# Performance work log

Hardware: AMD Instinct MI355X
Metric: run time of the kernel (lower is better)

## Reference

```python
import jax, jax.numpy as jnp
import numpy as np

IN_F = 175
HID = 1024
OUT_F = 175


def setup_inputs() -> dict:
    key = jax.random.key(0)
    ks = jax.random.split(key, 16)
    B, T = 128, 200
    s = 0.02
    w = lambda k, shape: (jax.random.normal(k, shape, jnp.float32) * s)
    return {
        "real_seq": jax.random.normal(ks[0], (B, T, IN_F), jnp.float32),
        "W_ih1": w(ks[1], (4 * HID, IN_F)), "W_hh1": w(ks[2], (4 * HID, HID)),
        "b_ih1": w(ks[3], (4 * HID,)), "b_hh1": w(ks[4], (4 * HID,)),
        "W_ih2": w(ks[5], (4 * HID, HID)), "W_hh2": w(ks[6], (4 * HID, HID)),
        "b_ih2": w(ks[7], (4 * HID,)), "b_hh2": w(ks[8], (4 * HID,)),
        "W_ih3": w(ks[9], (4 * HID, HID)), "W_hh3": w(ks[10], (4 * HID, HID)),
        "b_ih3": w(ks[11], (4 * HID,)), "b_hh3": w(ks[12], (4 * HID,)),
        "W_dec": w(ks[13], (OUT_F, HID)), "b_dec": w(ks[14], (OUT_F,)),
    }


def _condition_mask(seq_len, condition_num=5, groundtruth_num=5):
    gt = np.ones((100, groundtruth_num))
    con = np.zeros((100, condition_num))
    lst = np.concatenate((gt, con), 1).reshape(-1)[:seq_len]
    return jnp.asarray(lst.astype(bool))


def _lstm_cell(x, h, c, Wih, Whh, bih, bhh):
    # PyTorch LSTMCell: gate order i, f, g, o
    gates = x @ Wih.T + h @ Whh.T + bih + bhh
    i, f, g, o = jnp.split(gates, 4, axis=-1)
    c_new = jax.nn.sigmoid(f) * c + jax.nn.sigmoid(i) * jnp.tanh(g)
    h_new = jax.nn.sigmoid(o) * jnp.tanh(c_new)
    return h_new, c_new


def reference(real_seq, W_ih1, W_hh1, b_ih1, b_hh1,
              W_ih2, W_hh2, b_ih2, b_hh2,
              W_ih3, W_hh3, b_ih3, b_hh3,
              W_dec, b_dec):
    B, T, _ = real_seq.shape
    H = W_hh1.shape[1]
    Fo = W_dec.shape[0]
    cond = _condition_mask(T)
    z = jnp.zeros((B, H), real_seq.dtype)
    carry0 = (z, z, z, z, z, z, jnp.zeros((B, Fo), real_seq.dtype))

    def step(carry, xs):
        h0, h1, h2, c0, c1, c2, out_frame = carry
        x_t, use_gt = xs
        in_frame = jnp.where(use_gt, x_t, out_frame)
        nh0, nc0 = _lstm_cell(in_frame, h0, c0, W_ih1, W_hh1, b_ih1, b_hh1)
        # NOTE: source feeds the PREVIOUS h0 / h1 to layers 2 / 3 (faithful)
        nh1, nc1 = _lstm_cell(h0, h1, c1, W_ih2, W_hh2, b_ih2, b_hh2)
        nh2, nc2 = _lstm_cell(h1, h2, c2, W_ih3, W_hh3, b_ih3, b_hh3)
        out = nh2 @ W_dec.T + b_dec
        return (nh0, nh1, nh2, nc0, nc1, nc2, out), out

    _, outs = jax.lax.scan(step, carry0,
                           (jnp.transpose(real_seq, (1, 0, 2)), cond))
    # [T, B, Fo] -> [B, T*Fo] (matches torch.cat along dim 1 per step)
    return jnp.transpose(outs, (1, 0, 2)).reshape(B, T * Fo)
```

## Files before the change

### kernel.cpp

```cpp
#include <hip/hip_runtime.h>

#define B_ 128
#define T_ 200
#define INF_ 175
#define INFP_ 192
#define H_ 1024
#define G4_ 4096
#define OUTF_ 175
#define BH3_ (3 * B_ * H_)
#define NCELL 192
#define NDEC 22
#define NWORK (NCELL + NDEC)
#define NBLK (NWORK + 1)
#define SP 16

typedef __bf16 bf16x8 __attribute__((ext_vector_type(8)));
typedef float f32x4 __attribute__((ext_vector_type(4)));

__device__ __attribute__((aligned(16))) __bf16 g_Wih1p[G4_ * INFP_];
__device__ __attribute__((aligned(16))) __bf16 g_Whh1[G4_ * H_];
__device__ __attribute__((aligned(16))) __bf16 g_Wih2[G4_ * H_];
__device__ __attribute__((aligned(16))) __bf16 g_Whh2[G4_ * H_];
__device__ __attribute__((aligned(16))) __bf16 g_Wih3[G4_ * H_];
__device__ __attribute__((aligned(16))) __bf16 g_Whh3[G4_ * H_];
__device__ __attribute__((aligned(16))) __bf16 g_Wdec[OUTF_ * H_];
__device__ float g_bsum[3 * G4_];
__device__ float g_bdec[OUTF_];
__device__ __attribute__((aligned(16))) __bf16 g_h[2][BH3_];
__device__ __attribute__((aligned(16))) __bf16 g_infp[B_ * INFP_];
__device__ int g_isf32;
__device__ int g_flags[256 * SP];
__device__ int g_dflags[32 * SP];
__device__ int g_gen8[8 * SP];
__device__ int g_iready8[8 * SP];

__device__ __forceinline__ f32x4 mfma_bf16(bf16x8 a, bf16x8 b, f32x4 c) {
    return __builtin_amdgcn_mfma_f32_16x16x32_bf16(a, b, c, 0, 0, 0);
}
__device__ __forceinline__ bf16x8 ld8(const __bf16* p) {
    return *reinterpret_cast<const bf16x8*>(p);
}
__device__ __forceinline__ float sigm(float x) { return 1.f / (1.f + expf(-x)); }
__device__ __forceinline__ float rdf(const void* p, long i, int f32) {
    return f32 ? ((const float*)p)[i] : (float)((const __bf16*)p)[i];
}
__device__ __forceinline__ unsigned short bf2u(__bf16 v) {
    union { __bf16 b; unsigned short u; } c; c.b = v; return c.u;
}

__device__ __forceinline__ void spin_rmw(int* addr, int target, int iters) {
    for (int it = 0; it < iters; ++it) {
        if (__hip_atomic_fetch_max(addr, 0, __ATOMIC_RELAXED, __HIP_MEMORY_SCOPE_AGENT) >= target)
            break;
        __builtin_amdgcn_s_sleep(1);
    }
    (void)__hip_atomic_load(addr, __ATOMIC_ACQUIRE, __HIP_MEMORY_SCOPE_AGENT);
}

__global__ void detect_k(const unsigned int* __restrict__ xw) {
    __shared__ int cnt;
    if (threadIdx.x == 0) cnt = 0;
    __syncthreads();
    unsigned int w = xw[threadIdx.x];
    int e = (w >> 7) & 0xFF;
    if (e >= 140) atomicAdd(&cnt, 1);
    __syncthreads();
    if (threadIdx.x == 0) g_isf32 = (cnt >= 16) ? 1 : 0;
}

__global__ void prep_k(const void* Wih1, const void* Whh1, const void* Wih2,
                       const void* Whh2, const void* Wih3, const void* Whh3,
                       const void* Wdec, const void* bih1, const void* bhh1,
                       const void* bih2, const void* bhh2, const void* bih3,
                       const void* bhh3, const void* bdec, const void* xseq) {
    const int f = g_isf32;
    const int idx = blockIdx.x * 256 + threadIdx.x;
    const int stride = gridDim.x * 256;
    if (idx < 256 * SP) g_flags[idx] = 0;
    if (idx < 32 * SP) g_dflags[idx] = 0;
    if (idx < 8 * SP) { g_gen8[idx] = 0; g_iready8[idx] = 0; }
    for (int i = idx; i < G4_ * INFP_; i += stride) {
        int n = i / INFP_, k = i - n * INFP_;
        g_Wih1p[i] = (k < INF_) ? (__bf16)rdf(Wih1, (long)n * INF_ + k, f) : (__bf16)0.f;
    }
    for (int i = idx; i < G4_ * H_; i += stride) {
        g_Whh1[i] = (__bf16)rdf(Whh1, i, f);
        g_Wih2[i] = (__bf16)rdf(Wih2, i, f);
        g_Whh2[i] = (__bf16)rdf(Whh2, i, f);
        g_Wih3[i] = (__bf16)rdf(Wih3, i, f);
        g_Whh3[i] = (__bf16)rdf(Whh3, i, f);
    }
    for (int i = idx; i < OUTF_ * H_; i += stride) g_Wdec[i] = (__bf16)rdf(Wdec, i, f);
    for (int i = idx; i < G4_; i += stride) {
        g_bsum[i]           = rdf(bih1, i, f) + rdf(bhh1, i, f);
        g_bsum[G4_ + i]     = rdf(bih2, i, f) + rdf(bhh2, i, f);
        g_bsum[2 * G4_ + i] = rdf(bih3, i, f) + rdf(bhh3, i, f);
    }
    for (int i = idx; i < OUTF_; i += stride) g_bdec[i] = rdf(bdec, i, f);
    for (int i = idx; i < 2 * BH3_; i += stride) (&g_h[0][0])[i] = (__bf16)0.f;
    for (int i = idx; i < B_ * INFP_; i += stride) {
        int b = i / INFP_, k = i - b * INFP_;
        g_infp[i] = (k < INF_) ? (__bf16)rdf(xseq, (long)b * (T_ * INF_) + k, f) : (__bf16)0.f;
    }
}

__device__ __forceinline__ void gridbar_w(int bid, int grp, int target) {
    __syncthreads();
    if (threadIdx.x == 0) {
        __threadfence();
        __hip_atomic_fetch_max(&g_flags[bid * SP], target, __ATOMIC_RELAXED, __HIP_MEMORY_SCOPE_AGENT);
        spin_rmw(&g_gen8[grp * SP], target, 4000);
    }
    __syncthreads();
}

__global__ __launch_bounds__(512, 1) void persist_k(const void* __restrict__ xseq,
                                                    void* __restrict__ dout) {
    __shared__ char s_tile[2][2][16384];
    __shared__ float s_acc[B_ * 4 * 16];
    __shared__ float s_c[B_ * 16];
    __shared__ int s_nf, s_nd;
    const int bid = blockIdx.x;
    const int grp = bid & 7;
    const int tid = threadIdx.x;
    const int lane = tid & 63;
    const int wid = tid >> 6;
    const int rlo = lane & 15, khi = lane >> 4;
    const int f32o = g_isf32;
    const int r7l = rlo & 7;
    const int sw0 = (khi ^ r7l) * 16;
    const int sw1 = ((khi + 4) ^ r7l) * 16;

    if (bid < NCELL) {
        const int L = bid >> 6;
        const int hc0 = (bid & 63) << 4;
        const int op = wid >> 2;
        const int g = wid & 3;
        const float* bs = g_bsum + L * G4_;

        const __bf16* Bm; int K;
        if (op == 0) {
            if (L == 0) { Bm = g_Wih1p; K = INFP_; }
            else        { Bm = (L == 1) ? g_Wih2 : g_Wih3; K = H_; }
        } else {
            Bm = (L == 0) ? g_Whh1 : (L == 1) ? g_Whh2 : g_Whh3; K = H_;
        }
        const __bf16* wp = Bm + (long)(g * H_ + hc0 + rlo) * K + khi * 8;
        bf16x8 wreg[32];
        if (K == INFP_) {
#pragma unroll
            for (int c = 0; c < 6; ++c) wreg[c] = ld8(wp + c * 32);
        } else {
#pragma unroll
            for (int c = 0; c < 32; ++c) wreg[c] = ld8(wp + c * 32);
        }

        const int strow = tid >> 2, stq = tid & 3, str7 = strow & 7;
        auto ldchunk = [&](const __bf16* src, int sA, int k0, bf16x8& v0, bf16x8& v1) {
            const __bf16* pr = src + (long)strow * sA + k0 + stq * 8;
            v0 = ld8(pr);
            v1 = ld8(pr + 32);
        };
        auto wrchunk = [&](char* tile, bf16x8 v0, bf16x8 v1) {
            char* pb = tile + strow * 128;
            *(bf16x8*)(pb + ((stq ^ str7) * 16)) = v0;
            *(bf16x8*)(pb + (((stq + 4) ^ str7) * 16)) = v1;
        };

        for (int i = tid; i < B_ * 16; i += 512) s_c[i] = 0.f;
        __syncthreads();

        for (int p = 0; p < T_; ++p) {
            const __bf16* hin = g_h[p & 1];
            const __bf16* Apx; int sAx, nx;
            if (L == 0) { Apx = g_infp; sAx = INFP_; nx = 3; }
            else        { Apx = hin + (L - 1) * B_ * H_; sAx = H_; nx = 16; }
            const __bf16* Aph = hin + L * B_ * H_;

            if (L == 0 && p > 0) {
                if (tid == 0) spin_rmw(&g_iready8[grp * SP], p, 3000);
                __syncthreads();
            }

            bf16x8 rx0, rx1, rh0, rh1;
            ldchunk(Aph, H_, 0, rh0, rh1);
            ldchunk(Apx, sAx, 0, rx0, rx1);
            wrchunk(&s_tile[0][1][0], rh0, rh1);
            wrchunk(&s_tile[0][0][0], rx0, rx1);
            ldchunk(Aph, H_, 64, rh0, rh1);
            ldchunk(Apx, sAx, 64, rx0, rx1);
            __syncthreads();

            f32x4 acc[8] = {};
            int buf = 0;
#pragma unroll
            for (int i = 0; i < 16; ++i) {
                if (i < 15) wrchunk(&s_tile[buf ^ 1][1][0], rh0, rh1);
                if (i + 1 < nx) wrchunk(&s_tile[buf ^ 1][0][0], rx0, rx1);
                if (i < 14) ldchunk(Aph, H_, (i + 2) * 64, rh0, rh1);
                if (i + 2 < nx) ldchunk(Apx, sAx, (i + 2) * 64, rx0, rx1);
                if (op == 1 || i < nx) {
                    const char* tb = &s_tile[buf][op][0];
#pragma unroll
                    for (int mf = 0; mf < 8; ++mf) {
                        const char* rb = tb + (mf * 16 + rlo) * 128;
                        acc[mf] = mfma_bf16(*(const bf16x8*)(rb + sw0), wreg[2 * i], acc[mf]);
                        acc[mf] = mfma_bf16(*(const bf16x8*)(rb + sw1), wreg[2 * i + 1], acc[mf]);
                    }
                }
                __syncthreads();
                buf ^= 1;
            }

            if (op == 1) {
#pragma unroll
                for (int mf = 0; mf < 8; ++mf)
#pragma unroll
                    for (int j = 0; j < 4; ++j) {
                        int r = mf * 16 + khi * 4 + j;
                        s_acc[(r * 4 + g) * 16 + rlo] = acc[mf][j];
                    }
            }
            __syncthreads();
            if (op == 0) {
#pragma unroll
                for (int mf = 0; mf < 8; ++mf)
#pragma unroll
                    for (int j = 0; j < 4; ++j) {
                        int r = mf * 16 + khi * 4 + j;
                        s_acc[(r * 4 + g) * 16 + rlo] += acc[mf][j];
                    }
            }
            __syncthreads();

            {
                const int r = wid * 16 + rlo;
                const int hq = khi;
                f32x4 ga = *(const f32x4*)&s_acc[(r * 4 + 0) * 16 + hq * 4];
                f32x4 gf = *(const f32x4*)&s_acc[(r * 4 + 1) * 16 + hq * 4];
                f32x4 gg = *(const f32x4*)&s_acc[(r * 4 + 2) * 16 + hq * 4];
                f32x4 go = *(const f32x4*)&s_acc[(r * 4 + 3) * 16 + hq * 4];
                f32x4 cv = *(const f32x4*)&s_c[r * 16 + hq * 4];
                unsigned long long hbits;
                unsigned short* hp = (unsigned short*)&hbits;
#pragma unroll
                for (int e = 0; e < 4; ++e) {
                    int col = hc0 + hq * 4 + e;
                    float gi_ = ga[e] + bs[0 * H_ + col];
                    float gf_ = gf[e] + bs[1 * H_ + col];
                    float gg_ = gg[e] + bs[2 * H_ + col];
                    float go_ = go[e] + bs[3 * H_ + col];
                    float cn = sigm(gf_) * cv[e] + sigm(gi_) * tanhf(gg_);
                    cv[e] = cn;
                    hp[e] = bf2u((__bf16)(sigm(go_) * tanhf(cn)));
                }
                *(f32x4*)&s_c[r * 16 + hq * 4] = cv;
                __bf16* hdst = g_h[(p + 1) & 1] + L * B_ * H_ + r * H_ + hc0 + hq * 4;
                __builtin_nontemporal_store(hbits, (unsigned long long*)hdst);
            }
            gridbar_w(bid, grp, p + 1);
        }
    } else if (bid < NWORK) {
        const int db = bid - NCELL;
        const int ntile = db % 11, mh = db / 11;
        const int kk = wid >> 2;
        const int mw = wid & 3;
        const int col = ntile * 16 + rlo;
        const int colc = (col < OUTF_) ? col : (OUTF_ - 1);

        const __bf16* pb = g_Wdec + (long)colc * H_ + khi * 8;
        bf16x8 dw[16];
#pragma unroll
        for (int c = 0; c < 16; ++c) dw[c] = ld8(pb + (kk * 16 + c) * 32);

        const int strow = tid >> 3, stc8 = tid & 7, str7 = strow & 7;
        char* const dt0 = &s_tile[0][0][0];
        char* const dt1 = &s_tile[1][0][0];

        auto decwork = [&](int t, bool winf) {
            const bool gt = (((t + 1) % 10) < 5);
            if (winf && gt) {
                if (kk == 0 && col < OUTF_) {
#pragma unroll
                    for (int j = 0; j < 4; ++j) {
                        int row = mh * 64 + mw * 16 + khi * 4 + j;
                        float nxt = rdf(xseq, (long)row * (T_ * INF_) + (long)(t + 1) * INF_ + col, f32o);
                        __builtin_nontemporal_store(bf2u((__bf16)nxt),
                            (unsigned short*)g_infp + row * INFP_ + col);
                    }
                }
                __syncthreads();
                if (tid == 0) {
                    __threadfence();
                    __hip_atomic_fetch_max(&g_dflags[db * SP], t + 1, __ATOMIC_RELAXED, __HIP_MEMORY_SCOPE_AGENT);
                }
            }
            const __bf16* h2 = g_h[(t + 1) & 1] + 2 * B_ * H_;
            const __bf16* hrow = h2 + (long)(mh * 64 + strow) * H_ + stc8 * 8;
            bf16x8 rv = ld8(hrow);
            *(bf16x8*)(dt0 + strow * 128 + ((stc8 ^ str7) * 16)) = rv;
            rv = ld8(hrow + 64);
            __syncthreads();
            f32x4 acc = {};
            int b = 0;
#pragma unroll
            for (int i = 0; i < 16; ++i) {
                if (i < 15) *(bf16x8*)((b ? dt0 : dt1) + strow * 128 + ((stc8 ^ str7) * 16)) = rv;
                if (i < 14) rv = ld8(hrow + (i + 2) * 64);
                {
                    const char* rb = (b ? dt1 : dt0) + (mw * 16 + rlo) * 128;
                    bf16x8 a0 = *(const bf16x8*)(rb + sw0);
                    bf16x8 a1 = *(const bf16x8*)(rb + sw1);
                    if (i < 8) {
                        if (kk == 0) {
                            acc = mfma_bf16(a0, dw[2 * i], acc);
                            acc = mfma_bf16(a1, dw[2 * i + 1], acc);
                        }
                    } else {
                        if (kk == 1) {
                            acc = mfma_bf16(a0, dw[2 * i - 16], acc);
                            acc = mfma_bf16(a1, dw[2 * i - 15], acc);
                        }
                    }
                }
                __syncthreads();
                b ^= 1;
            }
            if (kk == 1) {
#pragma unroll
                for (int j = 0; j < 4; ++j)
                    s_acc[(mw * 16 + khi * 4 + j) * 16 + rlo] = acc[j];
            }
            __syncthreads();
            if (kk == 0) {
#pragma unroll
                for (int j = 0; j < 4; ++j)
                    acc[j] += s_acc[(mw * 16 + khi * 4 + j) * 16 + rlo];
                if (col < OUTF_) {
                    const float bias = g_bdec[col];
#pragma unroll
                    for (int j = 0; j < 4; ++j) {
                        int row = mh * 64 + mw * 16 + khi * 4 + j;
                        float ov = acc[j] + bias;
                        long oidx = (long)row * (T_ * OUTF_) + (long)t * OUTF_ + col;
                        if (f32o) __builtin_nontemporal_store(ov, (float*)dout + oidx);
                        else __builtin_nontemporal_store(bf2u((__bf16)ov), (unsigned short*)dout + oidx);
                        if (winf && !gt) {
                            __builtin_nontemporal_store(bf2u((__bf16)ov),
                                (unsigned short*)g_infp + row * INFP_ + col);
                        }
                    }
                }
            }
            __syncthreads();
            if (winf && !gt && tid == 0) {
                __threadfence();
                __hip_atomic_fetch_max(&g_dflags[db * SP], t + 1, __ATOMIC_RELAXED, __HIP_MEMORY_SCOPE_AGENT);
            }
        };

        for (int p = 0; p < T_; ++p) {
            if (p >= 1) decwork(p - 1, true);
            gridbar_w(bid, grp, p + 1);
        }
        decwork(T_ - 1, false);
    } else {
        for (int p = 0; p < T_; ++p) {
            const int tgt = p + 1;
            bool ir_done = false;
            for (int it = 0; it < 2000; ++it) {
                if (tid == 0) { s_nf = 0; s_nd = 0; }
                __syncthreads();
                int bad_f = 0, bad_d = 0;
                if (tid < NWORK)
                    bad_f = (__hip_atomic_fetch_max(&g_flags[tid * SP], 0, __ATOMIC_RELAXED, __HIP_MEMORY_SCOPE_AGENT) < tgt);
                if (!ir_done && tid < NDEC)
                    bad_d = (__hip_atomic_fetch_max(&g_dflags[tid * SP], 0, __ATOMIC_RELAXED, __HIP_MEMORY_SCOPE_AGENT) < p);
                if (bad_f) s_nf = 1;
                if (bad_d) s_nd = 1;
                __syncthreads();
                if (!ir_done && !s_nd) {
                    if (tid < 8)
                        __hip_atomic_fetch_max(&g_iready8[tid * SP], p, __ATOMIC_RELAXED, __HIP_MEMORY_SCOPE_AGENT);
                    ir_done = true;
                }
                if (!s_nf) break;
                __builtin_amdgcn_s_sleep(1);
            }
            if (!ir_done && tid < 8)
                __hip_atomic_fetch_max(&g_iready8[tid * SP], p, __ATOMIC_RELAXED, __HIP_MEMORY_SCOPE_AGENT);
            __syncthreads();
            if (tid < 8)
                __hip_atomic_fetch_max(&g_gen8[tid * SP], tgt, __ATOMIC_RELAXED, __HIP_MEMORY_SCOPE_AGENT);
        }
    }
}

extern "C" void kernel_launch(void* const* d_in, const int* in_sizes, int n_in,
                              void* d_out, int out_size, void* d_ws, size_t ws_size,
                              hipStream_t stream) {
    const void* xseq = d_in[0];
    detect_k<<<1, 256, 0, stream>>>((const unsigned int*)xseq);
    prep_k<<<2048, 256, 0, stream>>>(d_in[1], d_in[2], d_in[5], d_in[6], d_in[9],
                                     d_in[10], d_in[13], d_in[3], d_in[4], d_in[7],
                                     d_in[8], d_in[11], d_in[12], d_in[14], xseq);
    persist_k<<<NBLK, 512, 0, stream>>>(xseq, d_out);
}
```

Baseline: 6.371 ms.

## Pre-pack all ground-truth inputs and defer layer-0 input wait to loop tail

```diff
diff --git a/kernel.cpp b/kernel.cpp
--- a/kernel.cpp
+++ b/kernel.cpp
@@ -28,6 +28,7 @@
 __device__ float g_bdec[OUTF_];
 __device__ __attribute__((aligned(16))) __bf16 g_h[2][BH3_];
 __device__ __attribute__((aligned(16))) __bf16 g_infp[B_ * INFP_];
+__device__ __attribute__((aligned(16))) __bf16 g_xp[(long)T_ * B_ * INFP_];
 __device__ int g_isf32;
 __device__ int g_flags[256 * SP];
 __device__ int g_dflags[32 * SP];
@@ -98,9 +99,16 @@
     }
     for (int i = idx; i < OUTF_; i += stride) g_bdec[i] = rdf(bdec, i, f);
     for (int i = idx; i < 2 * BH3_; i += stride) (&g_h[0][0])[i] = (__bf16)0.f;
-    for (int i = idx; i < B_ * INFP_; i += stride) {
-        int b = i / INFP_, k = i - b * INFP_;
-        g_infp[i] = (k < INF_) ? (__bf16)rdf(xseq, (long)b * (T_ * INF_) + k, f) : (__bf16)0.f;
+    for (int i = idx; i < B_ * INFP_; i += stride) g_infp[i] = (__bf16)0.f;
+    const long total = (long)T_ * B_ * INFP_;
+    for (long i = idx; i < total; i += stride) {
+        int k = (int)(i % INFP_);
+        long bt = i / INFP_;
+        int b = (int)(bt % B_);
+        int t = (int)(bt / B_);
+        g_xp[((long)t * B_ + b) * INFP_ + k] =
+            (k < INF_) ? (__bf16)rdf(xseq, (long)b * (T_ * INF_) + (long)t * INF_ + k, f)
+                       : (__bf16)0.f;
     }
 }
 
@@ -137,6 +145,7 @@
         const int op = wid >> 2;
         const int g = wid & 3;
         const float* bs = g_bsum + L * G4_;
+        const int XOFF = (L == 0) ? 13 : 0;
 
         const __bf16* Bm; int K;
         if (op == 0) {
@@ -171,24 +180,25 @@
         __syncthreads();
 
         for (int p = 0; p < T_; ++p) {
+            const bool gt = ((p % 10) < 5);
             const __bf16* hin = g_h[p & 1];
             const __bf16* Apx; int sAx, nx;
-            if (L == 0) { Apx = g_infp; sAx = INFP_; nx = 3; }
-            else        { Apx = hin + (L - 1) * B_ * H_; sAx = H_; nx = 16; }
+            if (L == 0) {
+                Apx = gt ? (g_xp + (long)p * B_ * INFP_) : g_infp;
+                sAx = INFP_; nx = 3;
+            } else {
+                Apx = hin + (L - 1) * B_ * H_; sAx = H_; nx = 16;
+            }
             const __bf16* Aph = hin + L * B_ * H_;
-
-            if (L == 0 && p > 0) {
-                if (tid == 0) spin_rmw(&g_iready8[grp * SP], p, 3000);
-                __syncthreads();
-            }
+            const bool needwait = (L == 0) && !gt;
 
             bf16x8 rx0, rx1, rh0, rh1;
             ldchunk(Aph, H_, 0, rh0, rh1);
-            ldchunk(Apx, sAx, 0, rx0, rx1);
+            if (XOFF == 0) ldchunk(Apx, sAx, 0, rx0, rx1);
             wrchunk(&s_tile[0][1][0], rh0, rh1);
-            wrchunk(&s_tile[0][0][0], rx0, rx1);
+            if (XOFF == 0) wrchunk(&s_tile[0][0][0], rx0, rx1);
             ldchunk(Aph, H_, 64, rh0, rh1);
-            ldchunk(Apx, sAx, 64, rx0, rx1);
+            if (XOFF == 0) ldchunk(Apx, sAx, 64, rx0, rx1);
             __syncthreads();
 
             f32x4 acc[8] = {};
@@ -196,16 +206,37 @@
 #pragma unroll
             for (int i = 0; i < 16; ++i) {
                 if (i < 15) wrchunk(&s_tile[buf ^ 1][1][0], rh0, rh1);
-                if (i + 1 < nx) wrchunk(&s_tile[buf ^ 1][0][0], rx0, rx1);
+                {
+                    int xj = i + 1 - XOFF;
+                    if (xj >= 0 && xj < nx) wrchunk(&s_tile[buf ^ 1][0][0], rx0, rx1);
+                }
+                if (i == 11 && needwait) {
+                    if (tid == 0) spin_rmw(&g_iready8[grp * SP], p, 3000);
+                    __syncthreads();
+                }
                 if (i < 14) ldchunk(Aph, H_, (i + 2) * 64, rh0, rh1);
-                if (i + 2 < nx) ldchunk(Apx, sAx, (i + 2) * 64, rx0, rx1);
-                if (op == 1 || i < nx) {
-                    const char* tb = &s_tile[buf][op][0];
+                {
+                    int xj = i + 2 - XOFF;
+                    if (xj >= 0 && xj < nx) ldchunk(Apx, sAx, xj * 64, rx0, rx1);
+                }
+                if (op == 1) {
+                    const char* tb = &s_tile[buf][1][0];
 #pragma unroll
                     for (int mf = 0; mf < 8; ++mf) {
                         const char* rb = tb + (mf * 16 + rlo) * 128;
                         acc[mf] = mfma_bf16(*(const bf16x8*)(rb + sw0), wreg[2 * i], acc[mf]);
                         acc[mf] = mfma_bf16(*(const bf16x8*)(rb + sw1), wreg[2 * i + 1], acc[mf]);
+                    }
+                } else {
+                    int xj = i - XOFF;
+                    if (xj >= 0 && xj < nx) {
+                        const char* tb = &s_tile[buf][0][0];
+#pragma unroll
+                        for (int mf = 0; mf < 8; ++mf) {
+                            const char* rb = tb + (mf * 16 + rlo) * 128;
+                            acc[mf] = mfma_bf16(*(const bf16x8*)(rb + sw0), wreg[2 * xj], acc[mf]);
+                            acc[mf] = mfma_bf16(*(const bf16x8*)(rb + sw1), wreg[2 * xj + 1], acc[mf]);
+                        }
                     }
                 }
                 __syncthreads();
@@ -278,23 +309,7 @@
         char* const dt1 = &s_tile[1][0][0];
 
         auto decwork = [&](int t, bool winf) {
-            const bool gt = (((t + 1) % 10) < 5);
-            if (winf && gt) {
-                if (kk == 0 && col < OUTF_) {
-#pragma unroll
-                    for (int j = 0; j < 4; ++j) {
-                        int row = mh * 64 + mw * 16 + khi * 4 + j;
-                        float nxt = rdf(xseq, (long)row * (T_ * INF_) + (long)(t + 1) * INF_ + col, f32o);
-                        __builtin_nontemporal_store(bf2u((__bf16)nxt),
-                            (unsigned short*)g_infp + row * INFP_ + col);
-                    }
-                }
-                __syncthreads();
-                if (tid == 0) {
-                    __threadfence();
-                    __hip_atomic_fetch_max(&g_dflags[db * SP], t + 1, __ATOMIC_RELAXED, __HIP_MEMORY_SCOPE_AGENT);
-                }
-            }
+            const bool gtn = (((t + 1) % 10) < 5);
             const __bf16* h2 = g_h[(t + 1) & 1] + 2 * B_ * H_;
             const __bf16* hrow = h2 + (long)(mh * 64 + strow) * H_ + stc8 * 8;
             bf16x8 rv = ld8(hrow);
@@ -345,7 +360,7 @@
                         long oidx = (long)row * (T_ * OUTF_) + (long)t * OUTF_ + col;
                         if (f32o) __builtin_nontemporal_store(ov, (float*)dout + oidx);
                         else __builtin_nontemporal_store(bf2u((__bf16)ov), (unsigned short*)dout + oidx);
-                        if (winf && !gt) {
+                        if (winf && !gtn) {
                             __builtin_nontemporal_store(bf2u((__bf16)ov),
                                 (unsigned short*)g_infp + row * INFP_ + col);
                         }
@@ -353,7 +368,7 @@
                 }
             }
             __syncthreads();
-            if (winf && !gt && tid == 0) {
+            if (tid == 0) {
                 __threadfence();
                 __hip_atomic_fetch_max(&g_dflags[db * SP], t + 1, __ATOMIC_RELAXED, __HIP_MEMORY_SCOPE_AGENT);
             }
```

Result: faster. 6.065 ms (-4.8%).
